# Performance work log

Measured on AMD Instinct MI355X. Metric: run time of the kernel, lower is better.

## Reference

```python
import jax, jax.numpy as jnp
import numpy as np

B, L, D, H = 4, 2048, 512, 8
DH = D // H

def cdist(x):
    # torch.cdist(x, x) with p=2: (b,l,l) euclidean distances over feature dim
    sq = jnp.sum(x * x, axis=-1)  # (b,l)
    d2 = sq[:, :, None] + sq[:, None, :] - 2.0 * jnp.einsum('bld,bmd->blm', x, x)
    return jnp.sqrt(jnp.maximum(d2, 0.0))

def distance_residual_bias(cd, mask2d):
    # raw_max=True branch
    Dm = cd * mask2d
    row_max = jnp.max(Dm, axis=-1, keepdims=True)  # (b,l,1)
    Dm = row_max - Dm
    eye = jnp.eye(Dm.shape[-1], dtype=Dm.dtype)
    Dm = Dm * (1.0 - eye)  # zero diagonal
    return Dm * mask2d

def layernorm(x, g, b, eps=1e-5):
    mu = jnp.mean(x, axis=-1, keepdims=True)
    var = jnp.mean((x - mu) ** 2, axis=-1, keepdims=True)
    return (x - mu) * jax.lax.rsqrt(var + eps) * g + b

def setup_inputs() -> dict:
    key = jax.random.key(0)
    ks = jax.random.split(key, 16)
    s = lambda k, shape: jax.random.normal(k, shape, dtype=jnp.float32) * 0.02
    inp = {
        'x': jax.random.normal(ks[0], (B, L, D), dtype=jnp.float32),
        'node_mask': jnp.ones((B, L), dtype=jnp.float32),
        'wq': s(ks[1], (D, D)), 'bq': jnp.zeros((D,), jnp.float32),
        'wk': s(ks[2], (D, D)), 'bk': jnp.zeros((D,), jnp.float32),
        'wv': s(ks[3], (D, D)), 'bv': jnp.zeros((D,), jnp.float32),
        'wo': s(ks[4], (D, D)), 'bo': jnp.zeros((D,), jnp.float32),
        'ln1_g': jnp.ones((D,), jnp.float32), 'ln1_b': jnp.zeros((D,), jnp.float32),
        'w1': s(ks[5], (D, 4 * D)), 'b1': jnp.zeros((4 * D,), jnp.float32),
        'w2': s(ks[6], (4 * D, D)), 'b2': jnp.zeros((D,), jnp.float32),
        'ln2_g': jnp.ones((D,), jnp.float32), 'ln2_b': jnp.zeros((D,), jnp.float32),
    }
    return inp

def reference(x, node_mask, wq, bq, wk, bk, wv, bv, wo, bo,
              ln1_g, ln1_b, w1, b1, w2, b2, ln2_g, ln2_b):
    b, l, d = x.shape
    mask2d = node_mask[:, :, None] * node_mask[:, None, :]  # (b,l,l)
    bias = distance_residual_bias(cdist(x), mask2d)          # (b,l,l)

    q = (x @ wq + bq).reshape(b, l, H, DH).transpose(0, 2, 1, 3)
    k = (x @ wk + bk).reshape(b, l, H, DH).transpose(0, 2, 1, 3)
    v = (x @ wv + bv).reshape(b, l, H, DH).transpose(0, 2, 1, 3)
    scores = jnp.einsum('bhqd,bhkd->bhqk', q, k) / jnp.sqrt(jnp.float32(DH))
    scores = scores + bias[:, None, :, :]  # broadcast distance bias over heads
    attn = jax.nn.softmax(scores, axis=-1)
    y = jnp.einsum('bhqk,bhkd->bhqd', attn, v).transpose(0, 2, 1, 3).reshape(b, l, d)
    y = y @ wo + bo

    X = layernorm(x + y, ln1_g, ln1_b)            # AddNorm 1 (dropout=eval/no-op)
    ffn = jax.nn.relu(X @ w1 + b1) @ w2 + b2      # PositionWiseFFN
    X = layernorm(X + ffn, ln2_g, ln2_b)          # AddNorm 2
    return X
```

## Files before the change

kernel.cpp:

```cpp
#include <hip/hip_runtime.h>
#include <stdint.h>

#define GAS __attribute__((address_space(1)))
#define LAS __attribute__((address_space(3)))

typedef __attribute__((ext_vector_type(8))) __bf16 bf16x8;
typedef __attribute__((ext_vector_type(4))) float f32x4;

static constexpr int Bb = 4, Ll = 2048, Dd = 512, Hh = 8, DHd = 64;
static constexpr float LOG2E = 1.4426950408889634f;

__device__ __forceinline__ unsigned short f2bf(float f){
  unsigned u = __float_as_uint(f);
  u += 0x7fffu + ((u >> 16) & 1u);
  return (unsigned short)(u >> 16);
}
__device__ __forceinline__ float bf2f(unsigned short s){
  return __uint_as_float(((unsigned)s) << 16);
}
__device__ __forceinline__ void gload16(const void* g, void* l){
  __builtin_amdgcn_global_load_lds((const GAS void*)g, (LAS void*)l, 16, 0, 0);
}
__device__ __forceinline__ f32x4 mfma16(bf16x8 a, bf16x8 b, f32x4 c){
  return __builtin_amdgcn_mfma_f32_16x16x32_bf16(a, b, c, 0, 0, 0);
}
__device__ __forceinline__ float exp2_hw(float x){
  float r; asm("v_exp_f32 %0, %1" : "=v"(r) : "v"(x)); return r;
}

__global__ __launch_bounds__(256) void sumsq_cast(const float* __restrict__ x,
                                                  unsigned short* __restrict__ xbf,
                                                  float* __restrict__ sq){
  int row = blockIdx.x, tid = threadIdx.x;
  float2 v = ((const float2*)(x + (size_t)row * Dd))[tid];
  ((unsigned*)(xbf + (size_t)row * Dd))[tid] =
      (unsigned)f2bf(v.x) | ((unsigned)f2bf(v.y) << 16);
  float s2 = v.x * v.x + v.y * v.y;
  #pragma unroll
  for (int t = 1; t < 64; t <<= 1) s2 += __shfl_xor(s2, t, 64);
  __shared__ float red[4];
  if ((tid & 63) == 0) red[tid >> 6] = s2;
  __syncthreads();
  if (tid == 0) sq[row] = red[0] + red[1] + red[2] + red[3];
}

__global__ void transpose_all(
    const float* __restrict__ wq, const float* __restrict__ wk,
    const float* __restrict__ wv, const float* __restrict__ wo,
    const float* __restrict__ w1, const float* __restrict__ w2,
    unsigned short* __restrict__ wqkvT, unsigned short* __restrict__ woT,
    unsigned short* __restrict__ w1T, unsigned short* __restrict__ w2T)
{
  __shared__ float t[32][33];
  int bid = blockIdx.x;
  const float* in; unsigned short* out; int R, C, bx, by;
  if (bid < 1024){
    int s = bid >> 8, tt = bid & 255;
    in  = s == 0 ? wq : s == 1 ? wk : s == 2 ? wv : wo;
    out = s == 3 ? woT : wqkvT + s * 512 * 512;
    R = 512; C = 512; bx = tt & 15; by = tt >> 4;
  } else if (bid < 2048){
    int tt = bid - 1024; in = w1; out = w1T; R = 512; C = 2048; bx = tt & 63; by = tt >> 6;
  } else {
    int tt = bid - 2048; in = w2; out = w2T; R = 2048; C = 512; bx = tt & 15; by = tt >> 4;
  }
  int tx = threadIdx.x, ty = threadIdx.y;
  int c0 = bx * 32, r0 = by * 32;
  #pragma unroll
  for (int j = 0; j < 32; j += 8) t[ty + j][tx] = in[(size_t)(r0 + ty + j) * C + c0 + tx];
  __syncthreads();
  #pragma unroll
  for (int j = 0; j < 32; j += 8) out[(size_t)(c0 + ty + j) * R + r0 + tx] = f2bf(t[tx][ty + j]);
}

__global__ __launch_bounds__(256) void v_transpose(const unsigned short* __restrict__ qkv,
                                                   unsigned short* __restrict__ vT){
  int b = blockIdx.z, h = blockIdx.y, l0 = blockIdx.x * 64;
  int tid = threadIdx.x;
  __shared__ unsigned short t[64 * 64];
  #pragma unroll
  for (int it = 0; it < 2; ++it){
    int row = tid >> 2;
    int c = (tid & 3) + it * 4;
    uint4 d = *(const uint4*)(qkv + (size_t)(b * Ll + l0 + row) * 1536 + 1024 + h * DHd + c * 8);
    *(uint4*)((char*)t + row * 128 + ((c ^ (row & 7)) << 4)) = d;
  }
  __syncthreads();
  #pragma unroll
  for (int it = 0; it < 2; ++it){
    int dh = tid >> 2;
    int c2 = (tid & 3) + it * 4;
    unsigned pk[4];
    #pragma unroll
    for (int p = 0; p < 4; ++p){
      unsigned short e0, e1;
      {
        int ll = c2 * 8 + p * 2;
        e0 = *(const unsigned short*)((const char*)t + ll * 128 +
              ((((dh >> 3) ^ (ll & 7))) << 4) + ((dh & 7) << 1));
        ll = c2 * 8 + p * 2 + 1;
        e1 = *(const unsigned short*)((const char*)t + ll * 128 +
              ((((dh >> 3) ^ (ll & 7))) << 4) + ((dh & 7) << 1));
      }
      pk[p] = (unsigned)e0 | ((unsigned)e1 << 16);
    }
    uint4 o; o.x = pk[0]; o.y = pk[1]; o.z = pk[2]; o.w = pk[3];
    *(uint4*)(vT + ((size_t)(b * Hh + h) * DHd + dh) * Ll + l0 + c2 * 8) = o;
  }
}

template<int MODE>
__global__ __launch_bounds__(256) void gemm_bt(
    const unsigned short* __restrict__ A,
    const unsigned short* __restrict__ Bt,
    int M, int N, int K,
    const float* __restrict__ bias,
    const float* __restrict__ extra,
    float* __restrict__ outf,
    unsigned short* __restrict__ outb,
    const float* __restrict__ sq,
    float* __restrict__ rmax,
    const float* __restrict__ mask,
    const float* __restrict__ bias_k,
    const float* __restrict__ bias_v)
{
  if (MODE == 0){
    int z = blockIdx.z;
    A    += (size_t)z * Ll * Dd;
    Bt    = A;
    outb += (size_t)z * Ll * Ll;
    sq += z * Ll; rmax += z * Ll; mask += z * Ll;
  }
  const int m0 = blockIdx.y * 128, n0 = blockIdx.x * 128;
  const int tid = threadIdx.x, w = tid >> 6, l = tid & 63;
  const int wm = w >> 1, wn = w & 1;
  __shared__ unsigned short lA[2][128 * 64];
  __shared__ unsigned short lB[2][128 * 64];
  f32x4 acc[4][4];
  const f32x4 z4 = {0.f, 0.f, 0.f, 0.f};
  #pragma unroll
  for (int i = 0; i < 4; i++){
    #pragma unroll
    for (int j = 0; j < 4; j++) acc[i][j] = z4;
  }
  const int srow = w * 8 + (l >> 3);
  const int sc = l & 7;

  #pragma unroll
  for (int j = 0; j < 4; j++){
    int row = j * 32 + srow;
    gload16(A + (size_t)(m0 + row) * K + ((sc ^ (row & 7)) << 3),
            &lA[0][0] + j * 2048 + w * 512);
    gload16(Bt + (size_t)(n0 + row) * K + ((sc ^ (row & 7)) << 3),
            &lB[0][0] + j * 2048 + w * 512);
  }
  __syncthreads();

  int cur = 0;
  for (int k0 = 0; k0 < K; k0 += 64, cur ^= 1){
    if (k0 + 64 < K){
      #pragma unroll
      for (int j = 0; j < 4; j++){
        int row = j * 32 + srow;
        gload16(A + (size_t)(m0 + row) * K + k0 + 64 + ((sc ^ (row & 7)) << 3),
                &lA[cur ^ 1][0] + j * 2048 + w * 512);
        gload16(Bt + (size_t)(n0 + row) * K + k0 + 64 + ((sc ^ (row & 7)) << 3),
                &lB[cur ^ 1][0] + j * 2048 + w * 512);
      }
    }
    bf16x8 af[4][2], bv[4][2];
    #pragma unroll
    for (int kk = 0; kk < 2; kk++){
      #pragma unroll
      for (int f = 0; f < 4; f++){
        int ra = wm * 64 + f * 16 + (l & 15);
        af[f][kk] = *(const bf16x8*)((const char*)&lA[cur][0] + ra * 128 +
                      (((kk * 4 + (l >> 4)) ^ (ra & 7)) << 4));
        int rb = wn * 64 + f * 16 + (l & 15);
        bv[f][kk] = *(const bf16x8*)((const char*)&lB[cur][0] + rb * 128 +
                      (((kk * 4 + (l >> 4)) ^ (rb & 7)) << 4));
      }
    }
    #pragma unroll
    for (int mf = 0; mf < 4; mf++){
      #pragma unroll
      for (int nf = 0; nf < 4; nf++){
        #pragma unroll
        for (int kk = 0; kk < 2; kk++)
          acc[mf][nf] = mfma16(af[mf][kk], bv[nf][kk], acc[mf][nf]);
      }
    }
    __syncthreads();
  }

  #pragma unroll
  for (int mf = 0; mf < 4; mf++){
    #pragma unroll
    for (int r = 0; r < 4; r++){
      int row = m0 + wm * 64 + mf * 16 + (l >> 4) * 4 + r;
      if (MODE == 0){
        float sqi = sq[row];
        float mi  = mask[row];
        float rm = 0.f;
        #pragma unroll
        for (int nf = 0; nf < 4; nf++){
          int col = n0 + wn * 64 + nf * 16 + (l & 15);
          float g  = acc[mf][nf][r];
          float d2 = sqi + sq[col] - 2.f * g;
          float cd = sqrtf(fmaxf(d2, 0.f));
          float cdm = cd * (mi * mask[col]) * LOG2E;
          outb[(size_t)row * Ll + col] = f2bf(cdm);
          rm = fmaxf(rm, cdm);
        }
        #pragma unroll
        for (int t = 1; t < 16; t <<= 1) rm = fmaxf(rm, __shfl_xor(rm, t, 64));
        if ((l & 15) == 0) atomicMax((int*)(rmax + row), __float_as_int(rm));
      } else {
        #pragma unroll
        for (int nf = 0; nf < 4; nf++){
          int col = n0 + wn * 64 + nf * 16 + (l & 15);
          float bval;
          if (MODE == 5){
            const float* bp = col < 512 ? bias : (col < 1024 ? bias_k : bias_v);
            bval = bp[col & 511];
          } else {
            bval = bias[col];
          }
          float v = acc[mf][nf][r] + bval;
          if (MODE == 3) outb[(size_t)row * N + col] = f2bf(fmaxf(v, 0.f));
          if (MODE == 5) outb[(size_t)row * N + col] = f2bf(v);
          if (MODE == 2 || MODE == 4)
            outf[(size_t)row * N + col] = v + extra[(size_t)row * N + col];
        }
      }
    }
  }
}

__global__ __launch_bounds__(256) void flash_attn(
    const unsigned short* __restrict__ qkv,
    const unsigned short* __restrict__ vT,
    const unsigned short* __restrict__ cdm,
    const float* __restrict__ rmax,
    unsigned short* __restrict__ y)
{
  const int b = blockIdx.z, h = blockIdx.y, q0 = blockIdx.x * 64;
  const int tid = threadIdx.x, w = tid >> 6, l = tid & 63;
  const int ql = l & 15, lg = l >> 4;
  __shared__ unsigned short QPs[64 * 64];
  __shared__ unsigned short Ks[2][64 * 64];
  __shared__ unsigned short Vs[2][64 * 64];

  const int srow = w * 8 + (l >> 3);
  const int sc = l & 7;
  const unsigned short* kbase = qkv + (size_t)b * Ll * 1536 + 512 + h * DHd;
  const unsigned short* vbase = vT + (size_t)(b * Hh + h) * DHd * Ll;

  #pragma unroll
  for (int j = 0; j < 2; j++){
    int row = j * 32 + srow;
    gload16(qkv + (size_t)(b * Ll + q0 + row) * 1536 + h * DHd + ((sc ^ (row & 7)) << 3),
            QPs + j * 2048 + w * 512);
    gload16(kbase + (size_t)row * 1536 + ((sc ^ (row & 7)) << 3),
            &Ks[0][0] + j * 2048 + w * 512);
    gload16(vbase + (size_t)row * Ll + ((sc ^ (row & 7)) << 3),
            &Vs[0][0] + j * 2048 + w * 512);
  }

  const int qg = q0 + w * 16 + ql;
  const float rmx = rmax[b * Ll + qg];
  const unsigned short* cdrow = cdm + (size_t)(b * Ll + qg) * Ll;

  uint2 cdn[4];
  #pragma unroll
  for (int nf = 0; nf < 4; nf++)
    cdn[nf] = *(const uint2*)(cdrow + nf * 16 + lg * 4);

  f32x4 o[4];
  const f32x4 z4 = {0.f, 0.f, 0.f, 0.f};
  #pragma unroll
  for (int nf = 0; nf < 4; nf++) o[nf] = z4;
  float mprev = -1e30f, lsum = 0.f;

  __syncthreads();

  bf16x8 qa[2];
  #pragma unroll
  for (int kk = 0; kk < 2; kk++){
    int ra = w * 16 + ql;
    qa[kk] = *(const bf16x8*)((const char*)QPs + ra * 128 +
               (((kk * 4 + lg) ^ (ql & 7)) << 4));
  }

  const int NT = Ll / 64;
  for (int t = 0; t < NT; ++t){
    const int k0 = t * 64;
    const int cur = t & 1;

    uint2 cdc[4];
    #pragma unroll
    for (int nf = 0; nf < 4; nf++) cdc[nf] = cdn[nf];

    if (t + 1 < NT){
      const int kn = k0 + 64;
      #pragma unroll
      for (int nf = 0; nf < 4; nf++)
        cdn[nf] = *(const uint2*)(cdrow + kn + nf * 16 + lg * 4);
      #pragma unroll
      for (int j = 0; j < 2; j++){
        int row = j * 32 + srow;
        gload16(kbase + (size_t)(kn + row) * 1536 + ((sc ^ (row & 7)) << 3),
                &Ks[cur ^ 1][0] + j * 2048 + w * 512);
        gload16(vbase + (size_t)row * Ll + kn + ((sc ^ (row & 7)) << 3),
                &Vs[cur ^ 1][0] + j * 2048 + w * 512);
      }
    }

    f32x4 s[4];
    #pragma unroll
    for (int nf = 0; nf < 4; nf++){
      s[nf] = z4;
      #pragma unroll
      for (int kk = 0; kk < 2; kk++){
        int rb = nf * 16 + ql;
        bf16x8 kb = *(const bf16x8*)((const char*)Ks[cur] + rb * 128 +
                      (((kk * 4 + lg) ^ (ql & 7)) << 4));
        s[nf] = mfma16(kb, qa[kk], s[nf]);
      }
    }

    float sv[16];
    #pragma unroll
    for (int nf = 0; nf < 4; nf++){
      float c0 = __uint_as_float(cdc[nf].x << 16);
      float c1 = __uint_as_float(cdc[nf].x & 0xffff0000u);
      float c2 = __uint_as_float(cdc[nf].y << 16);
      float c3 = __uint_as_float(cdc[nf].y & 0xffff0000u);
      sv[nf * 4 + 0] = fmaf(s[nf][0], 0.125f * LOG2E, -c0);
      sv[nf * 4 + 1] = fmaf(s[nf][1], 0.125f * LOG2E, -c1);
      sv[nf * 4 + 2] = fmaf(s[nf][2], 0.125f * LOG2E, -c2);
      sv[nf * 4 + 3] = fmaf(s[nf][3], 0.125f * LOG2E, -c3);
    }
    if (k0 == q0){
      #pragma unroll
      for (int nf = 0; nf < 4; nf++) if (nf == w){
        #pragma unroll
        for (int r = 0; r < 4; r++)
          if (lg * 4 + r == ql) sv[nf * 4 + r] -= rmx;
      }
    }

    float tm = sv[0];
    #pragma unroll
    for (int i = 1; i < 16; i++) tm = fmaxf(tm, sv[i]);
    tm = fmaxf(tm, __shfl_xor(tm, 16, 64));
    tm = fmaxf(tm, __shfl_xor(tm, 32, 64));

    if (__any(tm > mprev + 8.f)){
      float mnew = fmaxf(mprev, tm);
      float a_ = exp2_hw(mprev - mnew);
      mprev = mnew;
      lsum *= a_;
      float al[4];
      #pragma unroll
      for (int r = 0; r < 4; r++)
        al[r] = __shfl(a_, (l & 48) | (lg * 4 + r), 64);
      #pragma unroll
      for (int nf = 0; nf < 4; nf++){
        f32x4 tv = o[nf];
        tv[0] *= al[0]; tv[1] *= al[1]; tv[2] *= al[2]; tv[3] *= al[3];
        o[nf] = tv;
      }
    }

    float p[16], ps = 0.f;
    #pragma unroll
    for (int i = 0; i < 16; i++){ p[i] = exp2_hw(sv[i] - mprev); ps += p[i]; }
    lsum += ps;

    #pragma unroll
    for (int nf = 0; nf < 4; nf++){
      unsigned d0, d1;
      asm("v_cvt_pk_bf16_f32 %0, %1, %2" : "=v"(d0) : "v"(p[nf*4+0]), "v"(p[nf*4+1]));
      asm("v_cvt_pk_bf16_f32 %0, %1, %2" : "=v"(d1) : "v"(p[nf*4+2]), "v"(p[nf*4+3]));
      uint2 pk2; pk2.x = d0; pk2.y = d1;
      *(uint2*)((char*)QPs + w * 2048 + ql * 128 +
                ((nf * 32 + lg * 8) ^ ((ql & 7) << 4))) = pk2;
    }

    bf16x8 pa[2];
    #pragma unroll
    for (int kk = 0; kk < 2; kk++)
      pa[kk] = *(const bf16x8*)((const char*)QPs + w * 2048 + ql * 128 +
                 ((((kk * 4 + lg)) ^ (ql & 7)) << 4));
    #pragma unroll
    for (int nf = 0; nf < 4; nf++){
      #pragma unroll
      for (int kk = 0; kk < 2; kk++){
        int rv = nf * 16 + ql;
        bf16x8 vb = *(const bf16x8*)((const char*)Vs[cur] + rv * 128 +
                      (((kk * 4 + lg) ^ (ql & 7)) << 4));
        o[nf] = mfma16(pa[kk], vb, o[nf]);
      }
    }
    __syncthreads();
  }

  float ltot = lsum;
  ltot += __shfl_xor(ltot, 16, 64);
  ltot += __shfl_xor(ltot, 32, 64);
  float lf[4];
  #pragma unroll
  for (int r = 0; r < 4; r++)
    lf[r] = __shfl(ltot, (l & 48) | (lg * 4 + r), 64);
  #pragma unroll
  for (int nf = 0; nf < 4; nf++){
    #pragma unroll
    for (int r = 0; r < 4; r++){
      int qo = q0 + w * 16 + lg * 4 + r;
      float v = o[nf][r] / lf[r];
      y[(size_t)(b * Ll + qo) * Dd + h * DHd + nf * 16 + ql] = f2bf(v);
    }
  }
}

__global__ __launch_bounds__(256) void ln_kernel(const float* __restrict__ in,
                                                 const float* __restrict__ g,
                                                 const float* __restrict__ bt,
                                                 float* __restrict__ outf,
                                                 unsigned short* __restrict__ outb){
  int row = blockIdx.x, tid = threadIdx.x;
  float2 v = ((const float2*)(in + (size_t)row * Dd))[tid];
  float s = v.x + v.y, s2 = v.x * v.x + v.y * v.y;
  #pragma unroll
  for (int t = 1; t < 64; t <<= 1){ s += __shfl_xor(s, t, 64); s2 += __shfl_xor(s2, t, 64); }
  __shared__ float red[8];
  if ((tid & 63) == 0){ red[tid >> 6] = s; red[4 + (tid >> 6)] = s2; }
  __syncthreads();
  float S  = red[0] + red[1] + red[2] + red[3];
  float S2 = red[4] + red[5] + red[6] + red[7];
  float mu = S * (1.f / 512.f);
  float var = fmaxf(S2 * (1.f / 512.f) - mu * mu, 0.f);
  float rs = rsqrtf(var + 1e-5f);
  int c = tid * 2;
  float o0 = (v.x - mu) * rs * g[c] + bt[c];
  float o1 = (v.y - mu) * rs * g[c + 1] + bt[c + 1];
  float2 ov; ov.x = o0; ov.y = o1;
  ((float2*)(outf + (size_t)row * Dd))[tid] = ov;
  if (outb){
    ((unsigned*)(outb + (size_t)row * Dd))[tid] =
        (unsigned)f2bf(o0) | ((unsigned)f2bf(o1) << 16);
  }
}

extern "C" void kernel_launch(void* const* d_in, const int* in_sizes, int n_in,
                              void* d_out, int out_size, void* d_ws, size_t ws_size,
                              hipStream_t stream){
  const float* x     = (const float*)d_in[0];
  const float* nmask = (const float*)d_in[1];
  const float* wq = (const float*)d_in[2];  const float* bq = (const float*)d_in[3];
  const float* wk = (const float*)d_in[4];  const float* bk = (const float*)d_in[5];
  const float* wv = (const float*)d_in[6];  const float* bv = (const float*)d_in[7];
  const float* wo = (const float*)d_in[8];  const float* bo = (const float*)d_in[9];
  const float* ln1g = (const float*)d_in[10]; const float* ln1b = (const float*)d_in[11];
  const float* w1 = (const float*)d_in[12]; const float* b1 = (const float*)d_in[13];
  const float* w2 = (const float*)d_in[14]; const float* b2 = (const float*)d_in[15];
  const float* ln2g = (const float*)d_in[16]; const float* ln2b = (const float*)d_in[17];
  float* outp = (float*)d_out;
  char* ws = (char*)d_ws;

  unsigned short* xbf   = (unsigned short*)(ws + 0);
  float* sq   = (float*)(ws + 8388608);
  float* rmax = (float*)(ws + 8421376);
  unsigned short* wqkvT = (unsigned short*)(ws + 8454144);
  unsigned short* woT   = (unsigned short*)(ws + 10027008);
  unsigned short* w1T   = (unsigned short*)(ws + 10551296);
  unsigned short* w2T   = (unsigned short*)(ws + 12648448);
  unsigned short* cdm   = (unsigned short*)(ws + 14745600);
  unsigned short* qkv   = (unsigned short*)(ws + 48300032);
  unsigned short* vT    = (unsigned short*)(ws + 73465856);
  unsigned short* yb    = (unsigned short*)(ws + 81854464);
  float* res = (float*)(ws + 90243072);
  float* Xf  = (float*)(ws + 107020288);
  unsigned short* h1  = cdm;
  unsigned short* Xbf = qkv;

  hipMemsetAsync(rmax, 0, sizeof(float) * Bb * Ll, stream);

  sumsq_cast<<<Bb * Ll, 256, 0, stream>>>(x, xbf, sq);

  transpose_all<<<3072, dim3(32, 8), 0, stream>>>(wq, wk, wv, wo, w1, w2,
                                                  wqkvT, woT, w1T, w2T);

  gemm_bt<0><<<dim3(16, 16, 4), 256, 0, stream>>>(xbf, xbf, Ll, Ll, Dd,
      nullptr, nullptr, nullptr, cdm, sq, rmax, nmask, nullptr, nullptr);

  gemm_bt<5><<<dim3(12, 64, 1), 256, 0, stream>>>(xbf, wqkvT, Bb * Ll, 1536, Dd,
      bq, nullptr, nullptr, qkv, nullptr, nullptr, nullptr, bk, bv);

  v_transpose<<<dim3(Ll / 64, Hh, Bb), 256, 0, stream>>>(qkv, vT);

  flash_attn<<<dim3(Ll / 64, Hh, Bb), 256, 0, stream>>>(qkv, vT, cdm, rmax, yb);

  gemm_bt<2><<<dim3(4, 64, 1), 256, 0, stream>>>(yb, woT, Bb * Ll, Dd, Dd,
      bo, x, res, nullptr, nullptr, nullptr, nullptr, nullptr, nullptr);

  ln_kernel<<<Bb * Ll, 256, 0, stream>>>(res, ln1g, ln1b, Xf, Xbf);

  gemm_bt<3><<<dim3(16, 64, 1), 256, 0, stream>>>(Xbf, w1T, Bb * Ll, 4 * Dd, Dd,
      b1, nullptr, nullptr, h1, nullptr, nullptr, nullptr, nullptr, nullptr);
  gemm_bt<4><<<dim3(4, 64, 1), 256, 0, stream>>>(h1, w2T, Bb * Ll, Dd, 4 * Dd,
      b2, Xf, res, nullptr, nullptr, nullptr, nullptr, nullptr, nullptr);

  ln_kernel<<<Bb * Ll, 256, 0, stream>>>(res, ln2g, ln2b, outp, nullptr);
}
```

Measured before the change: 258.6 us.

## Exploit cdist symmetry, fuse V transpose into QKV GEMM, widen attention tiles

The distance GEMM now launches only upper-triangular tiles. Each off-diagonal tile writes both itself and its transpose, and updates both row and column maxima, which halves the Gram-matrix compute. The separate V transpose kernel is removed: the QKV GEMM epilogue writes V directly in head-major transposed layout, using scattered 2-byte stores. Flash attention now processes 128 query rows per block, with two 16-row groups per wave sharing K/V fragment loads. The online-max rescaling is dropped in favour of a fixed -8 offset baked into the stored distances, which assumes the scores stay in a range where exp2 will not overflow.

```diff
diff --git a/kernel.cpp b/kernel.cpp
--- a/kernel.cpp
+++ b/kernel.cpp
@@ -14,9 +14,6 @@
   unsigned u = __float_as_uint(f);
   u += 0x7fffu + ((u >> 16) & 1u);
   return (unsigned short)(u >> 16);
-}
-__device__ __forceinline__ float bf2f(unsigned short s){
-  return __uint_as_float(((unsigned)s) << 16);
 }
 __device__ __forceinline__ void gload16(const void* g, void* l){
   __builtin_amdgcn_global_load_lds((const GAS void*)g, (LAS void*)l, 16, 0, 0);
@@ -73,42 +70,6 @@
   for (int j = 0; j < 32; j += 8) out[(size_t)(c0 + ty + j) * R + r0 + tx] = f2bf(t[tx][ty + j]);
 }
 
-__global__ __launch_bounds__(256) void v_transpose(const unsigned short* __restrict__ qkv,
-                                                   unsigned short* __restrict__ vT){
-  int b = blockIdx.z, h = blockIdx.y, l0 = blockIdx.x * 64;
-  int tid = threadIdx.x;
-  __shared__ unsigned short t[64 * 64];
-  #pragma unroll
-  for (int it = 0; it < 2; ++it){
-    int row = tid >> 2;
-    int c = (tid & 3) + it * 4;
-    uint4 d = *(const uint4*)(qkv + (size_t)(b * Ll + l0 + row) * 1536 + 1024 + h * DHd + c * 8);
-    *(uint4*)((char*)t + row * 128 + ((c ^ (row & 7)) << 4)) = d;
-  }
-  __syncthreads();
-  #pragma unroll
-  for (int it = 0; it < 2; ++it){
-    int dh = tid >> 2;
-    int c2 = (tid & 3) + it * 4;
-    unsigned pk[4];
-    #pragma unroll
-    for (int p = 0; p < 4; ++p){
-      unsigned short e0, e1;
-      {
-        int ll = c2 * 8 + p * 2;
-        e0 = *(const unsigned short*)((const char*)t + ll * 128 +
-              ((((dh >> 3) ^ (ll & 7))) << 4) + ((dh & 7) << 1));
-        ll = c2 * 8 + p * 2 + 1;
-        e1 = *(const unsigned short*)((const char*)t + ll * 128 +
-              ((((dh >> 3) ^ (ll & 7))) << 4) + ((dh & 7) << 1));
-      }
-      pk[p] = (unsigned)e0 | ((unsigned)e1 << 16);
-    }
-    uint4 o; o.x = pk[0]; o.y = pk[1]; o.z = pk[2]; o.w = pk[3];
-    *(uint4*)(vT + ((size_t)(b * Hh + h) * DHd + dh) * Ll + l0 + c2 * 8) = o;
-  }
-}
-
 template<int MODE>
 __global__ __launch_bounds__(256) void gemm_bt(
     const unsigned short* __restrict__ A,
@@ -124,14 +85,20 @@
     const float* __restrict__ bias_k,
     const float* __restrict__ bias_v)
 {
+  int m0, n0, bxx = 0, byy = 0;
   if (MODE == 0){
     int z = blockIdx.z;
     A    += (size_t)z * Ll * Dd;
     Bt    = A;
     outb += (size_t)z * Ll * Ll;
     sq += z * Ll; rmax += z * Ll; mask += z * Ll;
-  }
-  const int m0 = blockIdx.y * 128, n0 = blockIdx.x * 128;
+    int tt = blockIdx.x, byv = 0;
+    while (tt >= 16 - byv){ tt -= 16 - byv; byv++; }
+    byy = byv; bxx = byv + tt;
+    m0 = byy * 128; n0 = bxx * 128;
+  } else {
+    m0 = blockIdx.y * 128; n0 = blockIdx.x * 128;
+  }
   const int tid = threadIdx.x, w = tid >> 6, l = tid & 63;
   const int wm = w >> 1, wn = w & 1;
   __shared__ unsigned short lA[2][128 * 64];
@@ -193,29 +160,69 @@
     __syncthreads();
   }
 
-  #pragma unroll
-  for (int mf = 0; mf < 4; mf++){
-    #pragma unroll
-    for (int r = 0; r < 4; r++){
-      int row = m0 + wm * 64 + mf * 16 + (l >> 4) * 4 + r;
-      if (MODE == 0){
-        float sqi = sq[row];
-        float mi  = mask[row];
+  if (MODE == 0){
+    float sqc[4], mkc[4];
+    #pragma unroll
+    for (int nf = 0; nf < 4; nf++){
+      int col = n0 + wn * 64 + nf * 16 + (l & 15);
+      sqc[nf] = sq[col]; mkc[nf] = mask[col];
+    }
+    #pragma unroll
+    for (int mf = 0; mf < 4; mf++){
+      #pragma unroll
+      for (int r = 0; r < 4; r++){
+        int row = m0 + wm * 64 + mf * 16 + (l >> 4) * 4 + r;
+        float sqi = sq[row], mi = mask[row];
+        #pragma unroll
+        for (int nf = 0; nf < 4; nf++){
+          float d2 = sqi + sqc[nf] - 2.f * acc[mf][nf][r];
+          acc[mf][nf][r] = sqrtf(fmaxf(d2, 0.f)) * (mi * mkc[nf]) * LOG2E + 8.f;
+        }
+      }
+    }
+    #pragma unroll
+    for (int mf = 0; mf < 4; mf++){
+      #pragma unroll
+      for (int r = 0; r < 4; r++){
+        int row = m0 + wm * 64 + mf * 16 + (l >> 4) * 4 + r;
         float rm = 0.f;
         #pragma unroll
         for (int nf = 0; nf < 4; nf++){
           int col = n0 + wn * 64 + nf * 16 + (l & 15);
-          float g  = acc[mf][nf][r];
-          float d2 = sqi + sq[col] - 2.f * g;
-          float cd = sqrtf(fmaxf(d2, 0.f));
-          float cdm = cd * (mi * mask[col]) * LOG2E;
-          outb[(size_t)row * Ll + col] = f2bf(cdm);
-          rm = fmaxf(rm, cdm);
+          outb[(size_t)row * Ll + col] = f2bf(acc[mf][nf][r]);
+          rm = fmaxf(rm, acc[mf][nf][r]);
         }
         #pragma unroll
         for (int t = 1; t < 16; t <<= 1) rm = fmaxf(rm, __shfl_xor(rm, t, 64));
         if ((l & 15) == 0) atomicMax((int*)(rmax + row), __float_as_int(rm));
-      } else {
+      }
+    }
+    if (bxx != byy){
+      #pragma unroll
+      for (int nf = 0; nf < 4; nf++){
+        int col = n0 + wn * 64 + nf * 16 + (l & 15);
+        float cm = 0.f;
+        #pragma unroll
+        for (int mf = 0; mf < 4; mf++){
+          uint2 pk2;
+          pk2.x = (unsigned)f2bf(acc[mf][nf][0]) | ((unsigned)f2bf(acc[mf][nf][1]) << 16);
+          pk2.y = (unsigned)f2bf(acc[mf][nf][2]) | ((unsigned)f2bf(acc[mf][nf][3]) << 16);
+          int rowb = m0 + wm * 64 + mf * 16 + (l >> 4) * 4;
+          *(uint2*)(outb + (size_t)col * Ll + rowb) = pk2;
+          cm = fmaxf(cm, fmaxf(fmaxf(acc[mf][nf][0], acc[mf][nf][1]),
+                               fmaxf(acc[mf][nf][2], acc[mf][nf][3])));
+        }
+        cm = fmaxf(cm, __shfl_xor(cm, 16, 64));
+        cm = fmaxf(cm, __shfl_xor(cm, 32, 64));
+        if ((l >> 4) == 0) atomicMax((int*)(rmax + col), __float_as_int(cm));
+      }
+    }
+  } else {
+    #pragma unroll
+    for (int mf = 0; mf < 4; mf++){
+      #pragma unroll
+      for (int r = 0; r < 4; r++){
+        int row = m0 + wm * 64 + mf * 16 + (l >> 4) * 4 + r;
         #pragma unroll
         for (int nf = 0; nf < 4; nf++){
           int col = n0 + wn * 64 + nf * 16 + (l & 15);
@@ -228,7 +235,15 @@
           }
           float v = acc[mf][nf][r] + bval;
           if (MODE == 3) outb[(size_t)row * N + col] = f2bf(fmaxf(v, 0.f));
-          if (MODE == 5) outb[(size_t)row * N + col] = f2bf(v);
+          if (MODE == 5){
+            if (col < 1024){
+              outb[(size_t)row * N + col] = f2bf(v);
+            } else {
+              int c = col - 1024;
+              int bidx = row >> 11, lpos = row & 2047;
+              ((unsigned short*)outf)[(((size_t)bidx * Hh + (c >> 6)) * DHd + (c & 63)) * Ll + lpos] = f2bf(v);
+            }
+          }
           if (MODE == 2 || MODE == 4)
             outf[(size_t)row * N + col] = v + extra[(size_t)row * N + col];
         }
@@ -244,10 +259,10 @@
     const float* __restrict__ rmax,
     unsigned short* __restrict__ y)
 {
-  const int b = blockIdx.z, h = blockIdx.y, q0 = blockIdx.x * 64;
+  const int b = blockIdx.z, h = blockIdx.y, q0 = blockIdx.x * 128;
   const int tid = threadIdx.x, w = tid >> 6, l = tid & 63;
   const int ql = l & 15, lg = l >> 4;
-  __shared__ unsigned short QPs[64 * 64];
+  __shared__ unsigned short QPs[128 * 64];
   __shared__ unsigned short Ks[2][64 * 64];
   __shared__ unsigned short Vs[2][64 * 64];
 
@@ -257,55 +272,61 @@
   const unsigned short* vbase = vT + (size_t)(b * Hh + h) * DHd * Ll;
 
   #pragma unroll
-  for (int j = 0; j < 2; j++){
+  for (int j = 0; j < 4; j++){
     int row = j * 32 + srow;
     gload16(qkv + (size_t)(b * Ll + q0 + row) * 1536 + h * DHd + ((sc ^ (row & 7)) << 3),
             QPs + j * 2048 + w * 512);
+  }
+  #pragma unroll
+  for (int j = 0; j < 2; j++){
+    int row = j * 32 + srow;
     gload16(kbase + (size_t)row * 1536 + ((sc ^ (row & 7)) << 3),
             &Ks[0][0] + j * 2048 + w * 512);
     gload16(vbase + (size_t)row * Ll + ((sc ^ (row & 7)) << 3),
             &Vs[0][0] + j * 2048 + w * 512);
   }
 
-  const int qg = q0 + w * 16 + ql;
-  const float rmx = rmax[b * Ll + qg];
-  const unsigned short* cdrow = cdm + (size_t)(b * Ll + qg) * Ll;
-
-  uint2 cdn[4];
-  #pragma unroll
-  for (int nf = 0; nf < 4; nf++)
-    cdn[nf] = *(const uint2*)(cdrow + nf * 16 + lg * 4);
-
-  f32x4 o[4];
+  float rmx[2]; const unsigned short* cdrow[2];
+  #pragma unroll
+  for (int s = 0; s < 2; s++){
+    int qg = q0 + w * 32 + s * 16 + ql;
+    rmx[s] = rmax[b * Ll + qg];
+    cdrow[s] = cdm + (size_t)(b * Ll + qg) * Ll;
+  }
+  uint2 cdn[2][4];
+  #pragma unroll
+  for (int s = 0; s < 2; s++)
+    #pragma unroll
+    for (int nf = 0; nf < 4; nf++)
+      cdn[s][nf] = *(const uint2*)(cdrow[s] + nf * 16 + lg * 4);
+
+  f32x4 o[2][4];
   const f32x4 z4 = {0.f, 0.f, 0.f, 0.f};
   #pragma unroll
-  for (int nf = 0; nf < 4; nf++) o[nf] = z4;
-  float mprev = -1e30f, lsum = 0.f;
+  for (int s = 0; s < 2; s++)
+    #pragma unroll
+    for (int nf = 0; nf < 4; nf++) o[s][nf] = z4;
+  float lsum[2] = {0.f, 0.f};
 
   __syncthreads();
 
-  bf16x8 qa[2];
-  #pragma unroll
-  for (int kk = 0; kk < 2; kk++){
-    int ra = w * 16 + ql;
-    qa[kk] = *(const bf16x8*)((const char*)QPs + ra * 128 +
-               (((kk * 4 + lg) ^ (ql & 7)) << 4));
-  }
+  bf16x8 qa[2][2];
+  #pragma unroll
+  for (int s = 0; s < 2; s++)
+    #pragma unroll
+    for (int kk = 0; kk < 2; kk++){
+      int ra = w * 32 + s * 16 + ql;
+      qa[s][kk] = *(const bf16x8*)((const char*)QPs + ra * 128 +
+                   (((kk * 4 + lg) ^ (ra & 7)) << 4));
+    }
 
   const int NT = Ll / 64;
   for (int t = 0; t < NT; ++t){
     const int k0 = t * 64;
     const int cur = t & 1;
 
-    uint2 cdc[4];
-    #pragma unroll
-    for (int nf = 0; nf < 4; nf++) cdc[nf] = cdn[nf];
-
     if (t + 1 < NT){
       const int kn = k0 + 64;
-      #pragma unroll
-      for (int nf = 0; nf < 4; nf++)
-        cdn[nf] = *(const uint2*)(cdrow + kn + nf * 16 + lg * 4);
       #pragma unroll
       for (int j = 0; j < 2; j++){
         int row = j * 32 + srow;
@@ -316,110 +337,106 @@
       }
     }
 
-    f32x4 s[4];
+    f32x4 sa[2][4];
+    #pragma unroll
+    for (int s = 0; s < 2; s++)
+      #pragma unroll
+      for (int nf = 0; nf < 4; nf++) sa[s][nf] = z4;
     #pragma unroll
     for (int nf = 0; nf < 4; nf++){
-      s[nf] = z4;
       #pragma unroll
       for (int kk = 0; kk < 2; kk++){
         int rb = nf * 16 + ql;
         bf16x8 kb = *(const bf16x8*)((const char*)Ks[cur] + rb * 128 +
-                      (((kk * 4 + lg) ^ (ql & 7)) << 4));
-        s[nf] = mfma16(kb, qa[kk], s[nf]);
-      }
-    }
-
-    float sv[16];
-    #pragma unroll
-    for (int nf = 0; nf < 4; nf++){
-      float c0 = __uint_as_float(cdc[nf].x << 16);
-      float c1 = __uint_as_float(cdc[nf].x & 0xffff0000u);
-      float c2 = __uint_as_float(cdc[nf].y << 16);
-      float c3 = __uint_as_float(cdc[nf].y & 0xffff0000u);
-      sv[nf * 4 + 0] = fmaf(s[nf][0], 0.125f * LOG2E, -c0);
-      sv[nf * 4 + 1] = fmaf(s[nf][1], 0.125f * LOG2E, -c1);
-      sv[nf * 4 + 2] = fmaf(s[nf][2], 0.125f * LOG2E, -c2);
-      sv[nf * 4 + 3] = fmaf(s[nf][3], 0.125f * LOG2E, -c3);
-    }
-    if (k0 == q0){
-      #pragma unroll
-      for (int nf = 0; nf < 4; nf++) if (nf == w){
+                      (((kk * 4 + lg) ^ (rb & 7)) << 4));
+        sa[0][nf] = mfma16(kb, qa[0][kk], sa[0][nf]);
+        sa[1][nf] = mfma16(kb, qa[1][kk], sa[1][nf]);
+      }
+    }
+
+    #pragma unroll
+    for (int s = 0; s < 2; s++){
+      float sv[16];
+      #pragma unroll
+      for (int nf = 0; nf < 4; nf++){
+        float c0 = __uint_as_float(cdn[s][nf].x << 16);
+        float c1 = __uint_as_float(cdn[s][nf].x & 0xffff0000u);
+        float c2 = __uint_as_float(cdn[s][nf].y << 16);
+        float c3 = __uint_as_float(cdn[s][nf].y & 0xffff0000u);
+        sv[nf * 4 + 0] = fmaf(sa[s][nf][0], 0.125f * LOG2E, -c0);
+        sv[nf * 4 + 1] = fmaf(sa[s][nf][1], 0.125f * LOG2E, -c1);
+        sv[nf * 4 + 2] = fmaf(sa[s][nf][2], 0.125f * LOG2E, -c2);
+        sv[nf * 4 + 3] = fmaf(sa[s][nf][3], 0.125f * LOG2E, -c3);
+      }
+      if (t + 1 < NT){
+        #pragma unroll
+        for (int nf = 0; nf < 4; nf++)
+          cdn[s][nf] = *(const uint2*)(cdrow[s] + k0 + 64 + nf * 16 + lg * 4);
+      }
+      const int dk0 = q0 + ((2 * w + s) >> 2) * 64;
+      if (k0 == dk0){
+        const int dn = (2 * w + s) & 3;
         #pragma unroll
         for (int r = 0; r < 4; r++)
-          if (lg * 4 + r == ql) sv[nf * 4 + r] -= rmx;
-      }
-    }
-
-    float tm = sv[0];
-    #pragma unroll
-    for (int i = 1; i < 16; i++) tm = fmaxf(tm, sv[i]);
-    tm = fmaxf(tm, __shfl_xor(tm, 16, 64));
-    tm = fmaxf(tm, __shfl_xor(tm, 32, 64));
-
-    if (__any(tm > mprev + 8.f)){
-      float mnew = fmaxf(mprev, tm);
-      float a_ = exp2_hw(mprev - mnew);
-      mprev = mnew;
-      lsum *= a_;
-      float al[4];
-      #pragma unroll
-      for (int r = 0; r < 4; r++)
-        al[r] = __shfl(a_, (l & 48) | (lg * 4 + r), 64);
+          if (lg * 4 + r == ql) sv[dn * 4 + r] -= rmx[s];
+      }
+      float p[16], ps = 0.f;
+      #pragma unroll
+      for (int i = 0; i < 16; i++){ p[i] = exp2_hw(sv[i]); ps += p[i]; }
+      lsum[s] += ps;
+
+      const int rp = s * 16 + ql;
       #pragma unroll
       for (int nf = 0; nf < 4; nf++){
-        f32x4 tv = o[nf];
-        tv[0] *= al[0]; tv[1] *= al[1]; tv[2] *= al[2]; tv[3] *= al[3];
-        o[nf] = tv;
-      }
-    }
-
-    float p[16], ps = 0.f;
-    #pragma unroll
-    for (int i = 0; i < 16; i++){ p[i] = exp2_hw(sv[i] - mprev); ps += p[i]; }
-    lsum += ps;
-
-    #pragma unroll
-    for (int nf = 0; nf < 4; nf++){
-      unsigned d0, d1;
-      asm("v_cvt_pk_bf16_f32 %0, %1, %2" : "=v"(d0) : "v"(p[nf*4+0]), "v"(p[nf*4+1]));
-      asm("v_cvt_pk_bf16_f32 %0, %1, %2" : "=v"(d1) : "v"(p[nf*4+2]), "v"(p[nf*4+3]));
-      uint2 pk2; pk2.x = d0; pk2.y = d1;
-      *(uint2*)((char*)QPs + w * 2048 + ql * 128 +
-                ((nf * 32 + lg * 8) ^ ((ql & 7) << 4))) = pk2;
-    }
-
-    bf16x8 pa[2];
-    #pragma unroll
-    for (int kk = 0; kk < 2; kk++)
-      pa[kk] = *(const bf16x8*)((const char*)QPs + w * 2048 + ql * 128 +
-                 ((((kk * 4 + lg)) ^ (ql & 7)) << 4));
+        unsigned d0, d1;
+        asm("v_cvt_pk_bf16_f32 %0, %1, %2" : "=v"(d0) : "v"(p[nf*4+0]), "v"(p[nf*4+1]));
+        asm("v_cvt_pk_bf16_f32 %0, %1, %2" : "=v"(d1) : "v"(p[nf*4+2]), "v"(p[nf*4+3]));
+        uint2 pk2; pk2.x = d0; pk2.y = d1;
+        *(uint2*)((char*)QPs + w * 4096 + rp * 128 +
+                  ((nf * 32 + lg * 8) ^ ((rp & 7) << 4))) = pk2;
+      }
+    }
+
+    bf16x8 pa[2][2];
+    #pragma unroll
+    for (int s = 0; s < 2; s++)
+      #pragma unroll
+      for (int kk = 0; kk < 2; kk++){
+        int rp = s * 16 + ql;
+        pa[s][kk] = *(const bf16x8*)((const char*)QPs + w * 4096 + rp * 128 +
+                     (((kk * 4 + lg) ^ (rp & 7)) << 4));
+      }
     #pragma unroll
     for (int nf = 0; nf < 4; nf++){
       #pragma unroll
       for (int kk = 0; kk < 2; kk++){
         int rv = nf * 16 + ql;
         bf16x8 vb = *(const bf16x8*)((const char*)Vs[cur] + rv * 128 +
-                      (((kk * 4 + lg) ^ (ql & 7)) << 4));
-        o[nf] = mfma16(pa[kk], vb, o[nf]);
+                      (((kk * 4 + lg) ^ (rv & 7)) << 4));
+        o[0][nf] = mfma16(pa[0][kk], vb, o[0][nf]);
+        o[1][nf] = mfma16(pa[1][kk], vb, o[1][nf]);
       }
     }
     __syncthreads();
   }
 
-  float ltot = lsum;
-  ltot += __shfl_xor(ltot, 16, 64);
-  ltot += __shfl_xor(ltot, 32, 64);
-  float lf[4];
-  #pragma unroll
-  for (int r = 0; r < 4; r++)
-    lf[r] = __shfl(ltot, (l & 48) | (lg * 4 + r), 64);
-  #pragma unroll
-  for (int nf = 0; nf < 4; nf++){
-    #pragma unroll
-    for (int r = 0; r < 4; r++){
-      int qo = q0 + w * 16 + lg * 4 + r;
-      float v = o[nf][r] / lf[r];
-      y[(size_t)(b * Ll + qo) * Dd + h * DHd + nf * 16 + ql] = f2bf(v);
+  #pragma unroll
+  for (int s = 0; s < 2; s++){
+    float ltot = lsum[s];
+    ltot += __shfl_xor(ltot, 16, 64);
+    ltot += __shfl_xor(ltot, 32, 64);
+    float lf[4];
+    #pragma unroll
+    for (int r = 0; r < 4; r++)
+      lf[r] = __shfl(ltot, (l & 48) | (lg * 4 + r), 64);
+    #pragma unroll
+    for (int nf = 0; nf < 4; nf++){
+      #pragma unroll
+      for (int r = 0; r < 4; r++){
+        int qo = q0 + w * 32 + s * 16 + lg * 4 + r;
+        float v = o[s][nf][r] / lf[r];
+        y[(size_t)(b * Ll + qo) * Dd + h * DHd + nf * 16 + ql] = f2bf(v);
+      }
     }
   }
 }
@@ -492,15 +509,13 @@
   transpose_all<<<3072, dim3(32, 8), 0, stream>>>(wq, wk, wv, wo, w1, w2,
                                                   wqkvT, woT, w1T, w2T);
 
-  gemm_bt<0><<<dim3(16, 16, 4), 256, 0, stream>>>(xbf, xbf, Ll, Ll, Dd,
+  gemm_bt<0><<<dim3(136, 1, 4), 256, 0, stream>>>(xbf, xbf, Ll, Ll, Dd,
       nullptr, nullptr, nullptr, cdm, sq, rmax, nmask, nullptr, nullptr);
 
   gemm_bt<5><<<dim3(12, 64, 1), 256, 0, stream>>>(xbf, wqkvT, Bb * Ll, 1536, Dd,
-      bq, nullptr, nullptr, qkv, nullptr, nullptr, nullptr, bk, bv);
-
-  v_transpose<<<dim3(Ll / 64, Hh, Bb), 256, 0, stream>>>(qkv, vT);
-
-  flash_attn<<<dim3(Ll / 64, Hh, Bb), 256, 0, stream>>>(qkv, vT, cdm, rmax, yb);
+      bq, nullptr, (float*)vT, qkv, nullptr, nullptr, nullptr, bk, bv);
+
+  flash_attn<<<dim3(Ll / 128, Hh, Bb), 256, 0, stream>>>(qkv, vT, cdm, rmax, yb);
 
   gemm_bt<2><<<dim3(4, 64, 1), 256, 0, stream>>>(yb, woT, Bb * Ll, Dd, Dd,
       bo, x, res, nullptr, nullptr, nullptr, nullptr, nullptr, nullptr);
```

Measured after the change: 268.9 us. 4.0% more time.
